# Kernel tuning notes

Hardware: AMD Instinct MI355X
Metric: run time of the kernel (lower is better)

Reference implementation:

```python
import jax, jax.numpy as jnp
import numpy as np

D_MODEL = 256
N_HEADS = 8
N_LEVELS = 4
N_POINTS = 4
DH = D_MODEL // N_HEADS
SHAPES = [(100, 150), (50, 75), (25, 38), (13, 19)]  # per-level (H, W)
BATCH = 2


def setup_inputs() -> dict:
    key = jax.random.key(0)
    ks = jax.random.split(key, 8)
    Lq = sum(h * w for h, w in SHAPES)  # 19947
    d = D_MODEL
    off_dim = N_HEADS * N_LEVELS * N_POINTS * 2
    aw_dim = N_HEADS * N_LEVELS * N_POINTS
    s = 1.0 / np.sqrt(d).astype(np.float32)
    lsi = np.concatenate([[0], np.cumsum([h * w for h, w in SHAPES])[:-1]])
    return {
        "query": jax.random.normal(ks[0], (BATCH, Lq, d), jnp.float32),
        "reference_points": jax.random.uniform(ks[1], (BATCH, Lq, N_LEVELS, 2), jnp.float32),
        "input_flatten": jax.random.normal(ks[2], (BATCH, Lq, d), jnp.float32),
        "input_spatial_shapes": jnp.array(SHAPES, dtype=jnp.int32),
        "input_level_start_index": jnp.array(lsi, dtype=jnp.int32),
        "W_samp": 0.01 * jax.random.normal(ks[3], (off_dim, d), jnp.float32),
        "b_samp": 0.1 * jax.random.normal(ks[4], (off_dim,), jnp.float32),
        "W_attn": s * jax.random.normal(ks[5], (aw_dim, d), jnp.float32),
        "b_attn": jnp.zeros((aw_dim,), jnp.float32),
        "W_val": s * jax.random.normal(ks[6], (d, d), jnp.float32),
        "b_val": jnp.zeros((d,), jnp.float32),
        "W_out": s * jax.random.normal(ks[7], (d, d), jnp.float32),
        "b_out": jnp.zeros((d,), jnp.float32),
    }


def _bilinear(v, grid, Hl, Wl):
    # v: [N, H, Hl*Wl, Dh] flattened level feature map per head
    # grid: [N, H, Q, P, 2] in [-1, 1]; align_corners=False, zero padding
    N, H, Q, P, _ = grid.shape
    Dh = v.shape[-1]
    x = (grid[..., 0] + 1.0) * 0.5 * Wl - 0.5
    y = (grid[..., 1] + 1.0) * 0.5 * Hl - 0.5
    x0 = jnp.floor(x)
    y0 = jnp.floor(y)
    lx = x - x0
    ly = y - y0
    x0i = x0.astype(jnp.int32)
    y0i = y0.astype(jnp.int32)

    def corner(xi, yi, w):
        valid = (xi >= 0) & (xi < Wl) & (yi >= 0) & (yi < Hl)
        idx = jnp.clip(yi, 0, Hl - 1) * Wl + jnp.clip(xi, 0, Wl - 1)
        g = jnp.take_along_axis(v, idx.reshape(N, H, Q * P, 1), axis=2)
        return g.reshape(N, H, Q, P, Dh) * (w * valid)[..., None]

    return (corner(x0i, y0i, (1 - lx) * (1 - ly))
            + corner(x0i + 1, y0i, lx * (1 - ly))
            + corner(x0i, y0i + 1, (1 - lx) * ly)
            + corner(x0i + 1, y0i + 1, lx * ly))


def _forward(query, ref, x, shapes, W_samp, b_samp, W_attn, b_attn, W_val, b_val, W_out, b_out):
    N, Lq, d = query.shape
    H, L, P, Dh = N_HEADS, N_LEVELS, N_POINTS, DH
    # value projection -> [N, H, S, Dh]
    value = (x @ W_val.T + b_val).reshape(N, -1, H, Dh).transpose(0, 2, 1, 3)
    off = (query @ W_samp.T + b_samp).reshape(N, Lq, H, L, P, 2)
    attw = jax.nn.softmax((query @ W_attn.T + b_attn).reshape(N, Lq, H, L * P), axis=-1)
    attw = attw.reshape(N, Lq, H, L, P).transpose(0, 2, 1, 3, 4)  # [N,H,Lq,L,P]
    # offset normalizer is (W, H) per level
    norm = jnp.array([[w, h] for h, w in shapes], dtype=query.dtype)  # [L, 2]
    loc = ref[:, :, None, :, None, :] + off / norm[None, None, None, :, None, :]
    grids = (2.0 * loc - 1.0).transpose(0, 2, 1, 3, 4, 5)  # [N,H,Lq,L,P,2]

    acc = jnp.zeros((N, Lq, H, Dh), query.dtype)
    start = 0
    for lvl, (Hl, Wl) in enumerate(shapes):
        v = value[:, :, start:start + Hl * Wl]  # [N,H,Hl*Wl,Dh]
        start += Hl * Wl
        samp = _bilinear(v, grids[:, :, :, lvl], Hl, Wl)  # [N,H,Lq,P,Dh]
        acc = acc + jnp.einsum('nhqpd,nhqp->nqhd', samp, attw[:, :, :, lvl])
    out = acc.reshape(N, Lq, H * Dh)
    return out @ W_out.T + b_out


def reference(query, reference_points, input_flatten, input_spatial_shapes,
              input_level_start_index, W_samp, b_samp, W_attn, b_attn,
              W_val, b_val, W_out, b_out):
    shapes = [(int(h), int(w)) for h, w in np.asarray(input_spatial_shapes)]
    return _forward(query, reference_points, input_flatten, shapes,
                    W_samp, b_samp, W_attn, b_attn, W_val, b_val, W_out, b_out)
```

## Files before the change

### kernel.cpp

```cpp
#include <hip/hip_runtime.h>
#include <hip/hip_bf16.h>

#define NB 2
#define LQ 19947
#define LV 19947
#define DM 256
#define NH 8
#define NL 4
#define NP 4
#define MROWS (NB*LQ)
#define MPAD  39936
#define QPB 2
#define CB_X 9984

__device__ __constant__ int c_lvlH[4] = {100, 50, 25, 13};
__device__ __constant__ int c_lvlW[4] = {150, 75, 38, 19};
__device__ __constant__ int c_lvlS[4] = {0, 15000, 18750, 19700};

typedef __attribute__((ext_vector_type(8))) short short8;
typedef __attribute__((ext_vector_type(4))) float f32x4;

__device__ __forceinline__ unsigned short f2bf(float f) {
  unsigned u = __float_as_uint(f);
  u += 0x7FFFu + ((u >> 16) & 1u);
  return (unsigned short)(u >> 16);
}
__device__ __forceinline__ unsigned pk2bf(float x, float y) {
  return (unsigned)f2bf(x) | ((unsigned)f2bf(y) << 16);
}
__device__ __forceinline__ float bfl(unsigned u) { return __uint_as_float(u << 16); }
__device__ __forceinline__ float bfh(unsigned u) { return __uint_as_float(u & 0xFFFF0000u); }

__global__ __launch_bounds__(256) void conv_all(
    const float* __restrict__ xin, const float* __restrict__ query,
    const float* __restrict__ Wv, const float* __restrict__ Wsamp,
    const float* __restrict__ Wattn, const float* __restrict__ Wout,
    const float* __restrict__ bsamp, const float* __restrict__ battn,
    unsigned short* __restrict__ xb, unsigned short* __restrict__ qb,
    unsigned short* __restrict__ wvb, unsigned short* __restrict__ wqb,
    unsigned short* __restrict__ wob, float* __restrict__ bsa)
{
  const int b = blockIdx.x, t = threadIdx.x;
  if (b == 2 * CB_X + 224) {
    bsa[t] = bsamp[t];
    if (t < 128) bsa[256 + t] = battn[t];
    return;
  }
  const float* src; unsigned short* dst; int base, ns;
  if (b < CB_X)            { src = xin;   dst = xb;          base = b * 1024;                ns = MROWS * 256; }
  else if (b < 2*CB_X)     { src = query; dst = qb;          base = (b - CB_X) * 1024;       ns = MROWS * 256; }
  else if (b < 2*CB_X+64)  { src = Wv;    dst = wvb;         base = (b - 2*CB_X) * 1024;     ns = 65536; }
  else if (b < 2*CB_X+128) { src = Wsamp; dst = wqb;         base = (b - 2*CB_X-64) * 1024;  ns = 65536; }
  else if (b < 2*CB_X+160) { src = Wattn; dst = wqb + 65536; base = (b - 2*CB_X-128) * 1024; ns = 32768; }
  else                     { src = Wout;  dst = wob;         base = (b - 2*CB_X-160) * 1024; ns = 65536; }
  const int i = base + t * 4;
  ushort4 o;
  if (i + 4 <= ns) {
    const float4 v = *(const float4*)(src + i);
    o.x = f2bf(v.x); o.y = f2bf(v.y); o.z = f2bf(v.z); o.w = f2bf(v.w);
  } else {
    float vs[4];
    #pragma unroll
    for (int j = 0; j < 4; ++j) vs[j] = (i + j < ns) ? src[i + j] : 0.f;
    o.x = f2bf(vs[0]); o.y = f2bf(vs[1]); o.z = f2bf(vs[2]); o.w = f2bf(vs[3]);
  }
  *(ushort4*)(dst + i) = o;
}

template<int OUT_BF16>
__device__ __forceinline__ void gemm_bres(
    unsigned short* Bs,
    const unsigned short* __restrict__ Ab,
    const unsigned short* __restrict__ Wb,
    const float* __restrict__ bias,
    void* __restrict__ Cp, int Nn, int colBase, int Mstore)
{
  const int t = threadIdx.x;
  const int w = t >> 6, l = t & 63;
  const int wr = w >> 1, wc = w & 1;
  const int rowBase = blockIdx.x * 128;

  #pragma unroll
  for (int r = 0; r < 16; ++r) {
    const int flat = r * 256 + t;
    const int col = flat >> 5;
    const int kc  = flat & 31;
    const short8 v = *(const short8*)(Wb + (size_t)(colBase + col) * 256 + kc * 8);
    const int dchunk = col * 32 + (kc ^ (col & 31));
    *(short8*)&Bs[dchunk * 8] = v;
  }
  __syncthreads();

  const f32x4 z = {0.f, 0.f, 0.f, 0.f};
  f32x4 acc[4][4];
  #pragma unroll
  for (int i = 0; i < 4; ++i)
    #pragma unroll
    for (int j = 0; j < 4; ++j) acc[i][j] = z;

  const int kb = l >> 4;
  int arow[4];
  #pragma unroll
  for (int i = 0; i < 4; ++i) arow[i] = rowBase + wr * 64 + i * 16 + (l & 15);
  int bcol[4], bsw[4];
  #pragma unroll
  for (int j = 0; j < 4; ++j) {
    bcol[j] = wc * 64 + j * 16 + (l & 15);
    bsw[j]  = bcol[j] & 31;
  }

  short8 a_cur[4], a_nxt[4];
  #pragma unroll
  for (int i = 0; i < 4; ++i)
    a_cur[i] = *(const short8*)(Ab + (size_t)arow[i] * 256 + kb * 8);

  #pragma unroll
  for (int ks = 0; ks < 8; ++ks) {
    if (ks < 7) {
      #pragma unroll
      for (int i = 0; i < 4; ++i)
        a_nxt[i] = *(const short8*)(Ab + (size_t)arow[i] * 256 + (ks + 1) * 32 + kb * 8);
    }
    short8 bf[4];
    #pragma unroll
    for (int j = 0; j < 4; ++j) {
      const int chunk = bcol[j] * 32 + ((ks * 4 + kb) ^ bsw[j]);
      bf[j] = *(const short8*)&Bs[chunk * 8];
    }
    #pragma unroll
    for (int i = 0; i < 4; ++i)
      #pragma unroll
      for (int j = 0; j < 4; ++j)
        acc[i][j] = __builtin_amdgcn_mfma_f32_16x16x32_bf16(bf[j], a_cur[i], acc[i][j], 0, 0, 0);
    #pragma unroll
    for (int i = 0; i < 4; ++i) a_cur[i] = a_nxt[i];
  }

  const int row0 = rowBase + wr * 64 + (l & 15);
  const int col0 = colBase + wc * 64 + (l >> 4) * 4;
  #pragma unroll
  for (int j = 0; j < 4; ++j) {
    const float4 bj = *(const float4*)(bias + col0 + j * 16);
    #pragma unroll
    for (int i = 0; i < 4; ++i) {
      const int row = row0 + i * 16;
      if (OUT_BF16) {
        uint2 st;
        st.x = pk2bf(acc[i][j][0] + bj.x, acc[i][j][1] + bj.y);
        st.y = pk2bf(acc[i][j][2] + bj.z, acc[i][j][3] + bj.w);
        *(uint2*)((unsigned short*)Cp + (size_t)row * Nn + col0 + j * 16) = st;
      } else if (row < Mstore) {
        *(float4*)((float*)Cp + (size_t)row * Nn + col0 + j * 16) =
            make_float4(acc[i][j][0] + bj.x, acc[i][j][1] + bj.y,
                        acc[i][j][2] + bj.z, acc[i][j][3] + bj.w);
      }
    }
  }
}

__global__ __launch_bounds__(256) void gemm_front(
    const unsigned short* __restrict__ xb, const unsigned short* __restrict__ qb,
    const unsigned short* __restrict__ wvb, const unsigned short* __restrict__ wqb,
    const float* __restrict__ b_val, const float* __restrict__ bsa,
    unsigned short* __restrict__ value, unsigned short* __restrict__ oc)
{
  __shared__ alignas(16) unsigned short Bs[128 * 256];
  const int y = blockIdx.y;
  if (y < 2)
    gemm_bres<1>(Bs, xb, wvb, b_val, value, 256, y * 128, MPAD);
  else
    gemm_bres<1>(Bs, qb, wqb, bsa, oc, 384, (y - 2) * 128, MPAD);
}

__global__ __launch_bounds__(256) void gemm_out(
    const unsigned short* __restrict__ accb, const unsigned short* __restrict__ wob,
    const float* __restrict__ b_out, float* __restrict__ out)
{
  __shared__ alignas(16) unsigned short Bs[128 * 256];
  gemm_bres<0>(Bs, accb, wob, b_out, out, 256, blockIdx.y * 128, MROWS);
}

__global__ __launch_bounds__(128) void msda_sample(
    const unsigned short* __restrict__ value,
    const float* __restrict__ refp,
    const unsigned short* __restrict__ oc,
    unsigned short* __restrict__ accb)
{
  __shared__ float s_aw[QPB][128];
  __shared__ float s_ref[QPB][8];
  __shared__ alignas(16) unsigned s_poff[QPB][NH][17][4];
  __shared__ alignas(16) float    s_pw[QPB][NH][17][4];

  const int t = threadIdx.x;
  const int bq0 = blockIdx.x * QPB;

  {
    const int q = t >> 6, i = t & 63;
    const int bq = bq0 + q;
    const unsigned pw = *(const unsigned*)(oc + (size_t)bq * 384 + 256 + i * 2);
    s_aw[q][i * 2 + 0] = bfl(pw);
    s_aw[q][i * 2 + 1] = bfh(pw);
    if (t < QPB * 8) {
      const int q2 = t >> 3, j = t & 7;
      s_ref[q2][j] = refp[(size_t)(bq0 + q2) * 8 + j];
    }
  }
  __syncthreads();

  if (t < QPB * NH) {
    const int q = t >> 3, h = t & 7;
    float* aw = &s_aw[q][h * 16];
    float m = aw[0];
    #pragma unroll
    for (int i = 1; i < 16; ++i) m = fmaxf(m, aw[i]);
    float e[16]; float s = 0.f;
    #pragma unroll
    for (int i = 0; i < 16; ++i) { e[i] = __expf(aw[i] - m); s += e[i]; }
    const float inv = 1.f / s;
    #pragma unroll
    for (int i = 0; i < 16; ++i) aw[i] = e[i] * inv;
  }
  __syncthreads();

  #pragma unroll
  for (int it = t; it < QPB * 128; it += 128) {
    const int q = it >> 7, rem = it & 127;
    const int h = rem >> 4, idx = rem & 15;
    const int l = idx >> 2;
    const int bq = bq0 + q;
    const unsigned po = *(const unsigned*)(oc + (size_t)bq * 384 + rem * 2);
    const int Hl = c_lvlH[l], Wl = c_lvlW[l], st = c_lvlS[l];
    const float x = s_ref[q][l * 2 + 0] * (float)Wl - 0.5f + bfl(po);
    const float y = s_ref[q][l * 2 + 1] * (float)Hl - 0.5f + bfh(po);
    const float aw = s_aw[q][rem];
    const float x0f = floorf(x), y0f = floorf(y);
    const float lx = x - x0f, ly = y - y0f;
    const int x0 = (int)x0f, y0 = (int)y0f;
    const float vx0 = (x0 >= 0 && x0 < Wl) ? 1.f : 0.f;
    const float vx1 = (x0 >= -1 && x0 < Wl - 1) ? 1.f : 0.f;
    const float vy0 = (y0 >= 0 && y0 < Hl) ? 1.f : 0.f;
    const float vy1 = (y0 >= -1 && y0 < Hl - 1) ? 1.f : 0.f;
    const int xc0 = min(max(x0, 0), Wl - 1);
    const int xc1 = min(max(x0 + 1, 0), Wl - 1);
    const int yc0 = min(max(y0, 0), Hl - 1);
    const int yc1 = min(max(y0 + 1, 0), Hl - 1);
    const int r0 = st + yc0 * Wl, r1 = st + yc1 * Wl;
    s_poff[q][h][idx][0] = (unsigned)(r0 + xc0) * 512u;
    s_poff[q][h][idx][1] = (unsigned)(r0 + xc1) * 512u;
    s_poff[q][h][idx][2] = (unsigned)(r1 + xc0) * 512u;
    s_poff[q][h][idx][3] = (unsigned)(r1 + xc1) * 512u;
    s_pw[q][h][idx][0] = (1.f - lx) * (1.f - ly) * aw * (vx0 * vy0);
    s_pw[q][h][idx][1] = lx * (1.f - ly) * aw * (vx1 * vy0);
    s_pw[q][h][idx][2] = (1.f - lx) * ly * aw * (vx0 * vy1);
    s_pw[q][h][idx][3] = lx * ly * aw * (vx1 * vy1);
  }
  __syncthreads();

  const int w = t >> 6;
  const int lane = t & 63;
  const int bq = bq0 + w;
  const int n = bq / LQ;
  const char* vbase = (const char*)value + (size_t)n * (LV * 512);
  const int h = lane >> 3;
  const int laneoff = h * 64 + (lane & 7) * 8;

  float a0 = 0.f, a1 = 0.f, a2 = 0.f, a3 = 0.f;
  #pragma unroll
  for (int idx = 0; idx < 16; ++idx) {
    const uint4  of = *(const uint4*)&s_poff[w][h][idx][0];
    const float4 wt = *(const float4*)&s_pw[w][h][idx][0];
    const uint2 p00 = *(const uint2*)(vbase + (of.x + laneoff));
    const uint2 p10 = *(const uint2*)(vbase + (of.y + laneoff));
    const uint2 p01 = *(const uint2*)(vbase + (of.z + laneoff));
    const uint2 p11 = *(const uint2*)(vbase + (of.w + laneoff));
    a0 += wt.x * bfl(p00.x) + wt.y * bfl(p10.x) + wt.z * bfl(p01.x) + wt.w * bfl(p11.x);
    a1 += wt.x * bfh(p00.x) + wt.y * bfh(p10.x) + wt.z * bfh(p01.x) + wt.w * bfh(p11.x);
    a2 += wt.x * bfl(p00.y) + wt.y * bfl(p10.y) + wt.z * bfl(p01.y) + wt.w * bfl(p11.y);
    a3 += wt.x * bfh(p00.y) + wt.y * bfh(p10.y) + wt.z * bfh(p01.y) + wt.w * bfh(p11.y);
  }
  ushort4 o;
  o.x = f2bf(a0); o.y = f2bf(a1); o.z = f2bf(a2); o.w = f2bf(a3);
  *(ushort4*)(accb + (size_t)bq * 256 + lane * 4) = o;
}

extern "C" void kernel_launch(void* const* d_in, const int* in_sizes, int n_in,
                              void* d_out, int out_size, void* d_ws, size_t ws_size,
                              hipStream_t stream) {
  const float* query  = (const float*)d_in[0];
  const float* refp   = (const float*)d_in[1];
  const float* xin    = (const float*)d_in[2];
  const float* W_samp = (const float*)d_in[5];
  const float* b_samp = (const float*)d_in[6];
  const float* W_attn = (const float*)d_in[7];
  const float* b_attn = (const float*)d_in[8];
  const float* W_val  = (const float*)d_in[9];
  const float* b_val  = (const float*)d_in[10];
  const float* W_out  = (const float*)d_in[11];
  const float* b_out  = (const float*)d_in[12];
  float* out = (float*)d_out;
  (void)in_sizes; (void)n_in; (void)out_size; (void)ws_size;

  char* ws = (char*)d_ws;
  unsigned short* value = (unsigned short*)(ws);
  unsigned short* qb    = (unsigned short*)(ws + 20447232);
  unsigned short* xb    = (unsigned short*)(ws + 40894464);
  unsigned short* accb  = xb;
  unsigned short* oc    = (unsigned short*)(ws + 61341696);
  unsigned short* wvb   = (unsigned short*)(ws + 92012544);
  unsigned short* wqb   = (unsigned short*)(ws + 92143616);
  unsigned short* wob   = (unsigned short*)(ws + 92340224);
  float*          bsa   = (float*)(ws + 92471296);

  hipLaunchKernelGGL(conv_all, dim3(2 * CB_X + 225), dim3(256), 0, stream,
                     xin, query, W_val, W_samp, W_attn, W_out, b_samp, b_attn,
                     xb, qb, wvb, wqb, wob, bsa);
  hipLaunchKernelGGL(gemm_front, dim3(312, 5), dim3(256), 0, stream,
                     xb, qb, wvb, wqb, b_val, bsa, value, oc);
  hipLaunchKernelGGL(msda_sample, dim3(MROWS / QPB), dim3(128), 0, stream,
                     value, refp, oc, accb);
  hipLaunchKernelGGL(gemm_out, dim3(312, 2), dim3(256), 0, stream,
                     accb, wob, b_out, out);
}
```

Measured before the change: 304.9 us.

## Fuse fp32-to-bf16 activation conversion into GEMMs with A-resident LDS tiles

The separate pass that converted the input and query activations to bf16 is removed. The front GEMM now reads fp32 activations directly, converts them while staging a 128-row A tile in LDS, and loops over all output column tiles with that tile resident. Weight fragments are streamed from global memory with a three-deep register prefetch instead of being staged in LDS. This cuts a full write and re-read of both activation tensors and their extra launch, in exchange for fewer blocks per GEMM and weight reads from global or L2 on every k-step.

```diff
diff --git a/kernel.cpp b/kernel.cpp
--- a/kernel.cpp
+++ b/kernel.cpp
@@ -11,7 +11,6 @@
 #define MROWS (NB*LQ)
 #define MPAD  39936
 #define QPB 2
-#define CB_X 9984
 
 __device__ __constant__ int c_lvlH[4] = {100, 50, 25, 13};
 __device__ __constant__ int c_lvlW[4] = {150, 75, 38, 19};
@@ -31,153 +30,160 @@
 __device__ __forceinline__ float bfl(unsigned u) { return __uint_as_float(u << 16); }
 __device__ __forceinline__ float bfh(unsigned u) { return __uint_as_float(u & 0xFFFF0000u); }
 
-__global__ __launch_bounds__(256) void conv_all(
-    const float* __restrict__ xin, const float* __restrict__ query,
+__global__ __launch_bounds__(256) void wconv(
     const float* __restrict__ Wv, const float* __restrict__ Wsamp,
     const float* __restrict__ Wattn, const float* __restrict__ Wout,
     const float* __restrict__ bsamp, const float* __restrict__ battn,
-    unsigned short* __restrict__ xb, unsigned short* __restrict__ qb,
     unsigned short* __restrict__ wvb, unsigned short* __restrict__ wqb,
     unsigned short* __restrict__ wob, float* __restrict__ bsa)
 {
   const int b = blockIdx.x, t = threadIdx.x;
-  if (b == 2 * CB_X + 224) {
+  if (b == 224) {
     bsa[t] = bsamp[t];
     if (t < 128) bsa[256 + t] = battn[t];
     return;
   }
-  const float* src; unsigned short* dst; int base, ns;
-  if (b < CB_X)            { src = xin;   dst = xb;          base = b * 1024;                ns = MROWS * 256; }
-  else if (b < 2*CB_X)     { src = query; dst = qb;          base = (b - CB_X) * 1024;       ns = MROWS * 256; }
-  else if (b < 2*CB_X+64)  { src = Wv;    dst = wvb;         base = (b - 2*CB_X) * 1024;     ns = 65536; }
-  else if (b < 2*CB_X+128) { src = Wsamp; dst = wqb;         base = (b - 2*CB_X-64) * 1024;  ns = 65536; }
-  else if (b < 2*CB_X+160) { src = Wattn; dst = wqb + 65536; base = (b - 2*CB_X-128) * 1024; ns = 32768; }
-  else                     { src = Wout;  dst = wob;         base = (b - 2*CB_X-160) * 1024; ns = 65536; }
-  const int i = base + t * 4;
+  const float* src; unsigned short* dst; int i;
+  if (b < 64)       { src = Wv;    dst = wvb;          i = (b * 256 + t) * 4; }
+  else if (b < 128) { src = Wsamp; dst = wqb;          i = ((b - 64) * 256 + t) * 4; }
+  else if (b < 160) { src = Wattn; dst = wqb + 65536;  i = ((b - 128) * 256 + t) * 4; }
+  else              { src = Wout;  dst = wob;          i = ((b - 160) * 256 + t) * 4; }
+  const float4 v = *(const float4*)(src + i);
   ushort4 o;
-  if (i + 4 <= ns) {
-    const float4 v = *(const float4*)(src + i);
-    o.x = f2bf(v.x); o.y = f2bf(v.y); o.z = f2bf(v.z); o.w = f2bf(v.w);
-  } else {
-    float vs[4];
-    #pragma unroll
-    for (int j = 0; j < 4; ++j) vs[j] = (i + j < ns) ? src[i + j] : 0.f;
-    o.x = f2bf(vs[0]); o.y = f2bf(vs[1]); o.z = f2bf(vs[2]); o.w = f2bf(vs[3]);
-  }
+  o.x = f2bf(v.x); o.y = f2bf(v.y); o.z = f2bf(v.z); o.w = f2bf(v.w);
   *(ushort4*)(dst + i) = o;
 }
 
-template<int OUT_BF16>
-__device__ __forceinline__ void gemm_bres(
-    unsigned short* Bs,
-    const unsigned short* __restrict__ Ab,
+template<int SRC_F32, int OUT_BF16, int NCT>
+__device__ __forceinline__ void gemm_ares(
+    unsigned short* As,
+    const void* __restrict__ Asrc,
     const unsigned short* __restrict__ Wb,
     const float* __restrict__ bias,
-    void* __restrict__ Cp, int Nn, int colBase, int Mstore)
+    void* __restrict__ Cp, int Nn, int rowBase, int readGuard, int storeGuard)
 {
   const int t = threadIdx.x;
+
+  #pragma unroll
+  for (int r = 0; r < 16; ++r) {
+    const int flat = r * 256 + t;
+    const int row = flat >> 5;
+    const int kc  = flat & 31;
+    const int grow = rowBase + row;
+    uint4 d;
+    if (SRC_F32) {
+      float4 v0 = make_float4(0.f,0.f,0.f,0.f), v1 = v0;
+      if (grow < readGuard) {
+        const float* g = (const float*)Asrc + (size_t)grow * 256 + kc * 8;
+        v0 = *(const float4*)g;
+        v1 = *(const float4*)(g + 4);
+      }
+      d.x = pk2bf(v0.x, v0.y); d.y = pk2bf(v0.z, v0.w);
+      d.z = pk2bf(v1.x, v1.y); d.w = pk2bf(v1.z, v1.w);
+    } else {
+      d = *(const uint4*)((const unsigned short*)Asrc + (size_t)grow * 256 + kc * 8);
+    }
+    *(uint4*)&As[(row * 32 + (kc ^ (row & 31))) * 8] = d;
+  }
+  __syncthreads();
+
   const int w = t >> 6, l = t & 63;
   const int wr = w >> 1, wc = w & 1;
-  const int rowBase = blockIdx.x * 128;
-
-  #pragma unroll
-  for (int r = 0; r < 16; ++r) {
-    const int flat = r * 256 + t;
-    const int col = flat >> 5;
-    const int kc  = flat & 31;
-    const short8 v = *(const short8*)(Wb + (size_t)(colBase + col) * 256 + kc * 8);
-    const int dchunk = col * 32 + (kc ^ (col & 31));
-    *(short8*)&Bs[dchunk * 8] = v;
-  }
-  __syncthreads();
-
-  const f32x4 z = {0.f, 0.f, 0.f, 0.f};
-  f32x4 acc[4][4];
-  #pragma unroll
-  for (int i = 0; i < 4; ++i)
-    #pragma unroll
-    for (int j = 0; j < 4; ++j) acc[i][j] = z;
-
-  const int kb = l >> 4;
-  int arow[4];
-  #pragma unroll
-  for (int i = 0; i < 4; ++i) arow[i] = rowBase + wr * 64 + i * 16 + (l & 15);
-  int bcol[4], bsw[4];
-  #pragma unroll
-  for (int j = 0; j < 4; ++j) {
-    bcol[j] = wc * 64 + j * 16 + (l & 15);
-    bsw[j]  = bcol[j] & 31;
-  }
-
-  short8 a_cur[4], a_nxt[4];
-  #pragma unroll
-  for (int i = 0; i < 4; ++i)
-    a_cur[i] = *(const short8*)(Ab + (size_t)arow[i] * 256 + kb * 8);
-
-  #pragma unroll
-  for (int ks = 0; ks < 8; ++ks) {
-    if (ks < 7) {
+  const int lm = l & 15, lk = l >> 4;
+
+  int arow[4], amask[4];
+  #pragma unroll
+  for (int i = 0; i < 4; ++i) {
+    arow[i]  = wr * 64 + i * 16 + lm;
+    amask[i] = arow[i] & 31;
+  }
+
+  #pragma unroll
+  for (int ct = 0; ct < NCT; ++ct) {
+    const int colBase = ct * 128;
+    const unsigned short* bp[4];
+    #pragma unroll
+    for (int j = 0; j < 4; ++j)
+      bp[j] = Wb + (size_t)(colBase + wc * 64 + j * 16 + lm) * 256 + lk * 8;
+
+    short8 Bf[3][4];
+    #pragma unroll
+    for (int d = 0; d < 3; ++d)
+      #pragma unroll
+      for (int j = 0; j < 4; ++j)
+        Bf[d][j] = *(const short8*)(bp[j] + d * 32);
+
+    f32x4 acc[4][4];
+    const f32x4 z = {0.f, 0.f, 0.f, 0.f};
+    #pragma unroll
+    for (int i = 0; i < 4; ++i)
+      #pragma unroll
+      for (int j = 0; j < 4; ++j) acc[i][j] = z;
+
+    #pragma unroll
+    for (int ks = 0; ks < 8; ++ks) {
+      short8 bcur[4];
+      #pragma unroll
+      for (int j = 0; j < 4; ++j) bcur[j] = Bf[ks % 3][j];
+      if (ks < 5) {
+        #pragma unroll
+        for (int j = 0; j < 4; ++j)
+          Bf[ks % 3][j] = *(const short8*)(bp[j] + (ks + 3) * 32);
+      }
+      short8 af[4];
       #pragma unroll
       for (int i = 0; i < 4; ++i)
-        a_nxt[i] = *(const short8*)(Ab + (size_t)arow[i] * 256 + (ks + 1) * 32 + kb * 8);
+        af[i] = *(const short8*)&As[(arow[i] * 32 + ((ks * 4 + lk) ^ amask[i])) * 8];
+      #pragma unroll
+      for (int i = 0; i < 4; ++i)
+        #pragma unroll
+        for (int j = 0; j < 4; ++j)
+          acc[i][j] = __builtin_amdgcn_mfma_f32_16x16x32_bf16(bcur[j], af[i], acc[i][j], 0, 0, 0);
     }
-    short8 bf[4];
+
+    const int row0 = rowBase + wr * 64 + lm;
+    const int col0 = colBase + wc * 64 + lk * 4;
     #pragma unroll
     for (int j = 0; j < 4; ++j) {
-      const int chunk = bcol[j] * 32 + ((ks * 4 + kb) ^ bsw[j]);
-      bf[j] = *(const short8*)&Bs[chunk * 8];
-    }
-    #pragma unroll
-    for (int i = 0; i < 4; ++i)
-      #pragma unroll
-      for (int j = 0; j < 4; ++j)
-        acc[i][j] = __builtin_amdgcn_mfma_f32_16x16x32_bf16(bf[j], a_cur[i], acc[i][j], 0, 0, 0);
-    #pragma unroll
-    for (int i = 0; i < 4; ++i) a_cur[i] = a_nxt[i];
-  }
-
-  const int row0 = rowBase + wr * 64 + (l & 15);
-  const int col0 = colBase + wc * 64 + (l >> 4) * 4;
-  #pragma unroll
-  for (int j = 0; j < 4; ++j) {
-    const float4 bj = *(const float4*)(bias + col0 + j * 16);
-    #pragma unroll
-    for (int i = 0; i < 4; ++i) {
-      const int row = row0 + i * 16;
-      if (OUT_BF16) {
-        uint2 st;
-        st.x = pk2bf(acc[i][j][0] + bj.x, acc[i][j][1] + bj.y);
-        st.y = pk2bf(acc[i][j][2] + bj.z, acc[i][j][3] + bj.w);
-        *(uint2*)((unsigned short*)Cp + (size_t)row * Nn + col0 + j * 16) = st;
-      } else if (row < Mstore) {
-        *(float4*)((float*)Cp + (size_t)row * Nn + col0 + j * 16) =
-            make_float4(acc[i][j][0] + bj.x, acc[i][j][1] + bj.y,
-                        acc[i][j][2] + bj.z, acc[i][j][3] + bj.w);
+      const float4 bj = *(const float4*)(bias + col0 + j * 16);
+      #pragma unroll
+      for (int i = 0; i < 4; ++i) {
+        const int row = row0 + i * 16;
+        if (OUT_BF16) {
+          uint2 st;
+          st.x = pk2bf(acc[i][j][0] + bj.x, acc[i][j][1] + bj.y);
+          st.y = pk2bf(acc[i][j][2] + bj.z, acc[i][j][3] + bj.w);
+          *(uint2*)((unsigned short*)Cp + (size_t)row * Nn + col0 + j * 16) = st;
+        } else if (row < storeGuard) {
+          *(float4*)((float*)Cp + (size_t)row * Nn + col0 + j * 16) =
+              make_float4(acc[i][j][0] + bj.x, acc[i][j][1] + bj.y,
+                          acc[i][j][2] + bj.z, acc[i][j][3] + bj.w);
+        }
       }
     }
   }
 }
 
-__global__ __launch_bounds__(256) void gemm_front(
-    const unsigned short* __restrict__ xb, const unsigned short* __restrict__ qb,
+__global__ __launch_bounds__(256, 2) void gemm_front(
+    const float* __restrict__ xin, const float* __restrict__ query,
     const unsigned short* __restrict__ wvb, const unsigned short* __restrict__ wqb,
     const float* __restrict__ b_val, const float* __restrict__ bsa,
     unsigned short* __restrict__ value, unsigned short* __restrict__ oc)
 {
-  __shared__ alignas(16) unsigned short Bs[128 * 256];
-  const int y = blockIdx.y;
-  if (y < 2)
-    gemm_bres<1>(Bs, xb, wvb, b_val, value, 256, y * 128, MPAD);
+  __shared__ alignas(16) unsigned short As[128 * 256];
+  const int rowBase = blockIdx.x * 128;
+  if (blockIdx.y == 0)
+    gemm_ares<1, 1, 2>(As, xin, wvb, b_val, value, 256, rowBase, MROWS, MPAD);
   else
-    gemm_bres<1>(Bs, qb, wqb, bsa, oc, 384, (y - 2) * 128, MPAD);
-}
-
-__global__ __launch_bounds__(256) void gemm_out(
+    gemm_ares<1, 1, 3>(As, query, wqb, bsa, oc, 384, rowBase, MROWS, MPAD);
+}
+
+__global__ __launch_bounds__(256, 2) void gemm_out(
     const unsigned short* __restrict__ accb, const unsigned short* __restrict__ wob,
     const float* __restrict__ b_out, float* __restrict__ out)
 {
-  __shared__ alignas(16) unsigned short Bs[128 * 256];
-  gemm_bres<0>(Bs, accb, wob, b_out, out, 256, blockIdx.y * 128, MROWS);
+  __shared__ alignas(16) unsigned short As[128 * 256];
+  gemm_ares<0, 0, 2>(As, accb, wob, b_out, out, 256, blockIdx.x * 128, MPAD, MROWS);
 }
 
 __global__ __launch_bounds__(128) void msda_sample(
@@ -302,22 +308,20 @@
 
   char* ws = (char*)d_ws;
   unsigned short* value = (unsigned short*)(ws);
-  unsigned short* qb    = (unsigned short*)(ws + 20447232);
-  unsigned short* xb    = (unsigned short*)(ws + 40894464);
-  unsigned short* accb  = xb;
-  unsigned short* oc    = (unsigned short*)(ws + 61341696);
-  unsigned short* wvb   = (unsigned short*)(ws + 92012544);
-  unsigned short* wqb   = (unsigned short*)(ws + 92143616);
-  unsigned short* wob   = (unsigned short*)(ws + 92340224);
-  float*          bsa   = (float*)(ws + 92471296);
-
-  hipLaunchKernelGGL(conv_all, dim3(2 * CB_X + 225), dim3(256), 0, stream,
-                     xin, query, W_val, W_samp, W_attn, W_out, b_samp, b_attn,
-                     xb, qb, wvb, wqb, wob, bsa);
-  hipLaunchKernelGGL(gemm_front, dim3(312, 5), dim3(256), 0, stream,
-                     xb, qb, wvb, wqb, b_val, bsa, value, oc);
+  unsigned short* oc    = (unsigned short*)(ws + 20447232);
+  unsigned short* accb  = (unsigned short*)(ws + 51118080);
+  unsigned short* wvb   = (unsigned short*)(ws + 71565312);
+  unsigned short* wqb   = (unsigned short*)(ws + 71696384);
+  unsigned short* wob   = (unsigned short*)(ws + 71892992);
+  float*          bsa   = (float*)(ws + 72024064);
+
+  hipLaunchKernelGGL(wconv, dim3(225), dim3(256), 0, stream,
+                     W_val, W_samp, W_attn, W_out, b_samp, b_attn,
+                     wvb, wqb, wob, bsa);
+  hipLaunchKernelGGL(gemm_front, dim3(312, 2), dim3(256), 0, stream,
+                     xin, query, wvb, wqb, b_val, bsa, value, oc);
   hipLaunchKernelGGL(msda_sample, dim3(MROWS / QPB), dim3(128), 0, stream,
                      value, refp, oc, accb);
-  hipLaunchKernelGGL(gemm_out, dim3(312, 2), dim3(256), 0, stream,
+  hipLaunchKernelGGL(gemm_out, dim3(312), dim3(256), 0, stream,
                      accb, wob, b_out, out);
 }
```

Result: slower. 338.4 us (+11.0%).
